# Kernel tuning notes

Hardware: AMD Instinct MI355X
Metric: run time of the kernel (lower is better)

The kernel has to match this reference:

```python
import jax, jax.numpy as jnp
import numpy as np

EPS = 1e-5

def _rms(t, w):
    # RMSNorm over last dim with learned scale w (broadcastable)
    return t * jax.lax.rsqrt(jnp.mean(t * t, axis=-1, keepdims=True) + EPS) * w

def setup_inputs() -> dict:
    key = jax.random.key(0)
    ks = jax.random.split(key, 8)
    B, S, D, H, HD, M = 2, 2048, 1024, 16, 64, 2
    E = H * HD
    sc = 0.02
    x = jax.random.normal(ks[0], (B, S, D), jnp.float32)
    attn_mask = jnp.zeros((S, S), jnp.float32)  # additive mask
    mod_ids = jax.random.randint(ks[1], (B, S), 0, M)
    Wq = jax.random.normal(ks[2], (M, D, E), jnp.float32) * sc
    Wk = jax.random.normal(ks[3], (M, D, E), jnp.float32) * sc
    Wv = jax.random.normal(ks[4], (M, D, E), jnp.float32) * sc
    Wo = jax.random.normal(ks[5], (M, E, D), jnp.float32) * sc
    qn_w = jnp.ones((M, HD), jnp.float32)
    kn_w = jnp.ones((M, HD), jnp.float32)
    attn_norm_w = jnp.ones((M, D), jnp.float32)
    return {"x": x, "attn_mask": attn_mask, "mod_ids": mod_ids,
            "Wq": Wq, "Wk": Wk, "Wv": Wv, "Wo": Wo,
            "qn_w": qn_w, "kn_w": kn_w, "attn_norm_w": attn_norm_w}

def reference(x, attn_mask, mod_ids, Wq, Wk, Wv, Wo, qn_w, kn_w, attn_norm_w):
    B, S, D = x.shape
    M = Wq.shape[0]
    HD = qn_w.shape[-1]
    E = Wq.shape[-1]
    H = E // HD
    msk = jax.nn.one_hot(mod_ids, M, dtype=x.dtype)  # [B,S,M] one-hot routing

    # modality-expert QKV projections: [M,B,S,E]
    q_m = jnp.einsum('bsd,mde->mbse', x, Wq).reshape(M, B, S, H, HD)
    k_m = jnp.einsum('bsd,mde->mbse', x, Wk).reshape(M, B, S, H, HD)
    v_m = jnp.einsum('bsd,mde->mbse', x, Wv)
    # per-modality, per-head QK RMSNorm
    q_m = _rms(q_m, qn_w[:, None, None, None, :]).reshape(M, B, S, E)
    k_m = _rms(k_m, kn_w[:, None, None, None, :]).reshape(M, B, S, E)

    # merge modalities (scatter by routing mask)
    q = jnp.einsum('bsm,mbse->bse', msk, q_m).reshape(B, S, H, HD)
    k = jnp.einsum('bsm,mbse->bse', msk, k_m).reshape(B, S, H, HD)
    v = jnp.einsum('bsm,mbse->bse', msk, v_m).reshape(B, S, H, HD)

    # standard multi-head attention
    scores = jnp.einsum('bqhd,bkhd->bhqk', q, k) / jnp.sqrt(jnp.asarray(HD, x.dtype))
    scores = scores + attn_mask  # additive mask broadcast over [B,H]
    attn = jax.nn.softmax(scores, axis=-1)
    ctx = jnp.einsum('bhqk,bkhd->bqhd', attn, v).reshape(B, S, E)
    attn_weights = attn.mean(axis=1)  # [B,S,S], averaged over heads

    # modality-expert output projection + RMSNorm, scatter-merge back
    o_m = jnp.einsum('bse,med->mbsd', ctx, Wo)
    o_m = _rms(o_m, attn_norm_w[:, None, None, :])
    out = jnp.einsum('bsm,mbsd->bsd', msk, o_m)
    return out, attn_weights
```

## Files before the change

kernel.cpp:

```cpp
#include <hip/hip_runtime.h>
#include <cstdint>

#define Bc  2
#define Sc  2048
#define Dc  1024
#define Ec  1024
#define Hc  16
#define HDc 64
#define TTc (Bc*Sc)
#define TILE_R 128
#define NTILES 36
#define EPSc 1e-5f
#define LOG2E 1.44269504f
#define C2    (0.125f*LOG2E)

typedef unsigned short u16;
using bf8   = __attribute__((ext_vector_type(8))) short;
using f32x4 = __attribute__((ext_vector_type(4))) float;
#define MFMA(a,b,c) __builtin_amdgcn_mfma_f32_16x16x32_bf16(a,b,c,0,0,0)

static __device__ __forceinline__ u16 f2b(float f){
    return (u16)((__float_as_uint(f) + 0x8000u) >> 16);
}
static __device__ __forceinline__ float b2f(u16 s){
    return __uint_as_float(((unsigned)s) << 16);
}
static __device__ __forceinline__ float ex2(float x){
    return __builtin_amdgcn_exp2f(x);
}
static __device__ __forceinline__ unsigned cvtpk(float a, float b){
    unsigned r;
    asm("v_cvt_pk_bf16_f32 %0, %1, %2" : "=v"(r) : "v"(a), "v"(b));
    return r;
}
union bfpack { unsigned u[4]; bf8 v; };
static __device__ __forceinline__ float max3f(float a, float b, float c){
    return fmaxf(fmaxf(a, b), c);
}
static __device__ __forceinline__ u16* swz(u16* base, int row, int col8){
    return base + row*64 + ((col8 ^ (row & 7)) << 3);
}
static __device__ __forceinline__ const u16* swzc(const u16* base, int row, int col8){
    return base + row*64 + ((col8 ^ (row & 7)) << 3);
}
typedef const __attribute__((address_space(1))) void* gp1;
typedef __attribute__((address_space(3))) void* lp3;
static __device__ __forceinline__ void gl16(const void* g, void* l){
    __builtin_amdgcn_global_load_lds((gp1)g, (lp3)l, 16, 0, 0);
}
static __device__ __forceinline__ int pinv(int lr){
    return (lr & 0x23) | ((lr & 0x10) >> 2) | ((lr & 0x0C) << 1);
}

__global__ void k_perm(const int* __restrict__ mod, int* __restrict__ perm,
                       int* __restrict__ tmeta, u16* __restrict__ zbuf)
{
    __shared__ int cnt[4], segstart[4];
    int t = threadIdx.x;
    for (int i = t; i < 2048; i += 256) zbuf[i] = 0;
    if (t < 4) cnt[t] = 0;
    __syncthreads();
    for (int i = t; i < TTc; i += 256){
        int b = i >> 11; int m = mod[i];
        atomicAdd(&cnt[b*2+m], 1);
    }
    __syncthreads();
    if (t == 0){
        int off = 0;
        for (int i = 0; i < 4; i++){
            segstart[i] = off;
            int pad = ((cnt[i] + TILE_R - 1)/TILE_R)*TILE_R;
            for (int tt = off/TILE_R; tt < (off+pad)/TILE_R; tt++) tmeta[tt] = i;
            off += pad;
        }
        for (int tt = off/TILE_R; tt < NTILES; tt++) tmeta[tt] = -1;
    }
    __syncthreads();
    if (t < 4) cnt[t] = 0;
    for (int i = t; i < NTILES*TILE_R; i += 256) perm[i] = -1;
    __syncthreads();
    for (int i = t; i < TTc; i += 256){
        int b = i >> 11, s = i & 2047; int m = mod[i];
        int r = atomicAdd(&cnt[b*2+m], 1);
        perm[segstart[b*2+m] + r] = s;
    }
}

__global__ __launch_bounds__(256) void k_prep(
    const float* __restrict__ x, const float* __restrict__ mask,
    u16* __restrict__ xb, u16* __restrict__ maskb)
{
    int bid = blockIdx.x;
    if (bid < 4096){
        int i = (bid*256 + threadIdx.x)*4;
        float4 v = *(const float4*)&x[i];
        ushort4 o;
        o.x = f2b(v.x); o.y = f2b(v.y); o.z = f2b(v.z); o.w = f2b(v.w);
        *(ushort4*)&xb[i] = o;
    } else {
        int i = ((bid-4096)*256 + threadIdx.x)*4;
        float4 v = *(const float4*)&mask[i];
        ushort4 o;
        o.x = f2b(v.x*LOG2E); o.y = f2b(v.y*LOG2E);
        o.z = f2b(v.z*LOG2E); o.w = f2b(v.w*LOG2E);
        *(ushort4*)&maskb[i] = o;
    }
}

__global__ __launch_bounds__(256) void k_tcvt(
    const float* __restrict__ s0, const float* __restrict__ s1,
    const float* __restrict__ s2, const float* __restrict__ s3,
    u16* __restrict__ d0, u16* __restrict__ d1,
    u16* __restrict__ d2, u16* __restrict__ d3)
{
    int wsel = blockIdx.z >> 1, m = blockIdx.z & 1;
    const float* src = (wsel==0?s0:wsel==1?s1:wsel==2?s2:s3) + (size_t)m*1048576;
    u16*       dst = (wsel==0?d0:wsel==1?d1:wsel==2?d2:d3) + (size_t)m*1048576;
    __shared__ float sh[32][33];
    int t = threadIdx.x;
    int i0 = blockIdx.x*32, j0 = blockIdx.y*32;
    {
        int i = t >> 3, j4 = (t & 7)*4;
        *(float4*)&sh[i][j4] = *(const float4*)&src[(size_t)(i0+i)*1024 + j0 + j4];
    }
    __syncthreads();
    {
        int j = t >> 3, i4 = (t & 7)*4;
        ushort4 o;
        o.x = f2b(sh[i4+0][j]); o.y = f2b(sh[i4+1][j]);
        o.z = f2b(sh[i4+2][j]); o.w = f2b(sh[i4+3][j]);
        *(ushort4*)&dst[(size_t)(j0+j)*1024 + i0 + i4] = o;
    }
}

__global__ __launch_bounds__(256) void k_qkv(
    const u16* __restrict__ xb, const u16* __restrict__ wqT,
    const u16* __restrict__ wkT, const u16* __restrict__ wvT,
    const int* __restrict__ perm, const int* __restrict__ tmeta,
    const float* __restrict__ qnw, const float* __restrict__ knw,
    const u16* __restrict__ zbuf,
    u16* __restrict__ qb, u16* __restrict__ kb, u16* __restrict__ vb)
{
    int meta = tmeta[blockIdx.y];
    if (meta < 0) return;
    int b = meta >> 1, m = meta & 1;
    const u16* W = (blockIdx.z==0 ? wqT : (blockIdx.z==1 ? wkT : wvT)) + (size_t)m*Ec*Dc;
    u16* outp    = (blockIdx.z==0 ? qb  : (blockIdx.z==1 ? kb  : vb));
    int c0 = blockIdx.x*128;
    int t = threadIdx.x, lane = t & 63, wv_ = t >> 6;
    int quad = lane >> 4, lc = lane & 15;

    __shared__ u16 at[128*64];
    __shared__ u16 bt[128*64];
    __shared__ int sperm[128];
    if (t < 128) sperm[t] = perm[blockIdx.y*128 + t];
    f32x4 acc[2][8];
    #pragma unroll
    for (int i=0;i<2;i++)
        #pragma unroll
        for (int j=0;j<8;j++) acc[i][j] = (f32x4){0.f,0.f,0.f,0.f};
    __syncthreads();

    int colsw = ((lane & 7) ^ (lane >> 3)) << 3;
    const u16* ab[4]; const u16* bb[4];
    #pragma unroll
    for (int i = 0; i < 4; i++){
        int row = wv_*32 + i*8 + (lane >> 3);
        int s_ = sperm[row];
        ab[i] = (s_ >= 0) ? (xb + ((size_t)(b*Sc + s_))*Dc + colsw) : zbuf;
        bb[i] = W + (size_t)(c0 + row)*Dc + colsw;
    }

    for (int d0 = 0; d0 < Dc; d0 += 64){
        #pragma unroll
        for (int i = 0; i < 4; i++){
            gl16(ab[i] + d0, &at[(wv_*4 + i)*512]);
            gl16(bb[i] + d0, &bt[(wv_*4 + i)*512]);
        }
        __syncthreads();
        #pragma unroll
        for (int ks = 0; ks < 2; ks++){
            bf8 a0 = *(const bf8*)swzc(at, wv_*32 + lc,      ks*4 + quad);
            bf8 a1 = *(const bf8*)swzc(at, wv_*32 + 16 + lc, ks*4 + quad);
            #pragma unroll
            for (int nb = 0; nb < 8; nb++){
                bf8 bb2 = *(const bf8*)swzc(bt, nb*16 + lc, ks*4 + quad);
                acc[0][nb] = MFMA(a0, bb2, acc[0][nb]);
                acc[1][nb] = MFMA(a1, bb2, acc[1][nb]);
            }
        }
        __syncthreads();
    }

    if (blockIdx.z < 2){
        const float* nw = (blockIdx.z==0 ? qnw : knw) + m*HDc;
        float cs = (blockIdx.z==0) ? C2 : 1.f;
        float w0 = nw[lc]*cs, w1 = nw[16+lc]*cs, w2 = nw[32+lc]*cs, w3 = nw[48+lc]*cs;
        #pragma unroll
        for (int mb = 0; mb < 2; mb++){
            #pragma unroll
            for (int r = 0; r < 4; r++){
                #pragma unroll
                for (int g = 0; g < 2; g++){
                    float ss = 0.f;
                    #pragma unroll
                    for (int j = 0; j < 4; j++){
                        float v2 = acc[mb][g*4+j][r];
                        ss += v2*v2;
                    }
                    ss += __shfl_xor(ss, 1, 64);
                    ss += __shfl_xor(ss, 2, 64);
                    ss += __shfl_xor(ss, 4, 64);
                    ss += __shfl_xor(ss, 8, 64);
                    float rs = rsqrtf(ss*(1.f/64.f) + EPSc);
                    acc[mb][g*4+0][r] *= rs*w0;
                    acc[mb][g*4+1][r] *= rs*w1;
                    acc[mb][g*4+2][r] *= rs*w2;
                    acc[mb][g*4+3][r] *= rs*w3;
                }
            }
        }
    }

    int h0 = c0 >> 6;
    #pragma unroll
    for (int mb = 0; mb < 2; mb++){
        #pragma unroll
        for (int r = 0; r < 4; r++){
            int row = wv_*32 + mb*16 + quad*4 + r;
            int s_ = sperm[row];
            if (s_ < 0) continue;
            #pragma unroll
            for (int nb = 0; nb < 8; nb++){
                int col = nb*16 + lc;
                int h = h0 + (col >> 6), hd = col & 63;
                outp[(((size_t)(b*Hc + h))*Sc + s_)*HDc + hd] = f2b(acc[mb][nb][r]);
            }
        }
    }
}

__global__ __launch_bounds__(256) void k_vt(const u16* __restrict__ vb,
                                            u16* __restrict__ vtb)
{
    __shared__ u16 sh[64][72];
    int t = threadIdx.x;
    int s0 = blockIdx.x*64, bh = blockIdx.y;
    {
        int rr = t >> 2, cc = (t & 3)*16;
        const u16* src = vb + ((size_t)bh*Sc + s0 + rr)*HDc + cc;
        *(uint4*)&sh[rr][cc]   = *(const uint4*)(src);
        *(uint4*)&sh[rr][cc+8] = *(const uint4*)(src+8);
    }
    __syncthreads();
    {
        int hd = t >> 2, sc = (t & 3)*16;
        u16 tmp[16];
        #pragma unroll
        for (int j = 0; j < 16; j++) tmp[j] = sh[sc+j][hd];
        u16* dst = vtb + ((size_t)bh*HDc + hd)*Sc + s0 + sc;
        *(uint4*)(dst)   = *(const uint4*)&tmp[0];
        *(uint4*)(dst+8) = *(const uint4*)&tmp[8];
    }
}

__global__ __launch_bounds__(256) void k_flash(
    const u16* __restrict__ qb, const u16* __restrict__ kb,
    const u16* __restrict__ vtb, const u16* __restrict__ maskb,
    float* __restrict__ pm, float* __restrict__ pl,
    u16* __restrict__ c0, u16* __restrict__ c1)
{
    int qs0 = blockIdx.x*64, h = blockIdx.y;
    int b = blockIdx.z >> 1, half = blockIdx.z & 1;
    u16* ctxh = half ? c1 : c0;
    int t = threadIdx.x, lane = t & 63, wv_ = t >> 6;
    int quad = lane >> 4, lc = lane & 15;
    __shared__ u16 kt[2][64*64];
    __shared__ u16 vt[2][64*64];
    const u16* qp  = qb  + ((size_t)(b*Hc+h))*Sc*HDc;
    const u16* kp  = kb  + ((size_t)(b*Hc+h))*Sc*HDc;
    const u16* vtp = vtb + ((size_t)(b*Hc+h))*HDc*Sc;
    const u16* mq  = maskb + (size_t)(qs0 + wv_*16 + lc)*Sc;
    bf8 aq[2];
    #pragma unroll
    for (int ks = 0; ks < 2; ks++)
        aq[ks] = *(const bf8*)(qp + (size_t)(qs0 + wv_*16 + lc)*HDc + ks*32 + quad*8);
    bfpack onep; onep.u[0] = onep.u[1] = onep.u[2] = onep.u[3] = 0x3F803F80u;
    bf8 ones = onep.v;
    float rm = -1.0e30f;
    f32x4 racc = (f32x4){0.f,0.f,0.f,0.f};
    f32x4 oacc[4];
    #pragma unroll
    for (int j=0;j<4;j++) oacc[j] = (f32x4){0.f,0.f,0.f,0.f};

    int lsub = lane >> 3;
    int colsw = ((lane & 7) ^ lsub) << 3;
    int lrA = wv_*16 + lsub, lrB = wv_*16 + 8 + lsub;
    const u16* kg0 = kp + (size_t)pinv(lrA)*HDc + colsw;
    const u16* kg1 = kp + (size_t)pinv(lrB)*HDc + colsw;
    const u16* vg0 = vtp + (size_t)lrA*Sc + colsw;
    const u16* vg1 = vtp + (size_t)lrB*Sc + colsw;
    int kdo0 = (wv_*16 + 0)*64, kdo1 = (wv_*16 + 8)*64;

    int kc0 = half*1024, kcend = kc0 + 1024;
    gl16(kg0 + (size_t)kc0*HDc, &kt[0][kdo0]);
    gl16(kg1 + (size_t)kc0*HDc, &kt[0][kdo1]);
    gl16(vg0 + kc0, &vt[0][kdo0]);
    gl16(vg1 + kc0, &vt[0][kdo1]);
    ushort4 mv[2][2];
    #pragma unroll
    for (int a1 = 0; a1 < 2; a1++)
        #pragma unroll
        for (int b1 = 0; b1 < 2; b1++)
            mv[a1][b1] = *(const ushort4*)(mq + kc0 + a1*32 + quad*8 + b1*4);
    __syncthreads();

    int cur = 0;
    for (int kc = kc0; kc < kcend; kc += 64){
        int nxt = (kc + 64 < kcend) ? kc + 64 : kc;
        gl16(kg0 + (size_t)nxt*HDc, &kt[cur^1][kdo0]);
        gl16(kg1 + (size_t)nxt*HDc, &kt[cur^1][kdo1]);
        gl16(vg0 + nxt, &vt[cur^1][kdo0]);
        gl16(vg1 + nxt, &vt[cur^1][kdo1]);
        ushort4 mvn[2][2];
        #pragma unroll
        for (int a1 = 0; a1 < 2; a1++)
            #pragma unroll
            for (int b1 = 0; b1 < 2; b1++)
                mvn[a1][b1] = *(const ushort4*)(mq + nxt + a1*32 + quad*8 + b1*4);

        const u16* ktc = kt[cur];
        const u16* vtc = vt[cur];
        f32x4 acc[4];
        #pragma unroll
        for (int j=0;j<4;j++) acc[j] = (f32x4){0.f,0.f,0.f,0.f};
        #pragma unroll
        for (int ks = 0; ks < 2; ks++){
            #pragma unroll
            for (int nb = 0; nb < 4; nb++){
                bf8 ak = *(const bf8*)swzc(ktc, nb*16 + lc, ks*4 + quad);
                acc[nb] = MFMA(ak, aq[ks], acc[nb]);
            }
        }
        float svv[4][4];
        #pragma unroll
        for (int a1 = 0; a1 < 2; a1++){
            #pragma unroll
            for (int b1 = 0; b1 < 2; b1++){
                int nb = 2*a1 + b1;
                #pragma unroll
                for (int r = 0; r < 4; r++){
                    u16 mraw = (r==0?mv[a1][b1].x:r==1?mv[a1][b1].y:
                                r==2?mv[a1][b1].z:mv[a1][b1].w);
                    svv[nb][r] = acc[nb][r] + b2f(mraw);
                }
            }
        }
        float m0_ = max3f(svv[0][0], svv[0][1], svv[0][2]);
        float m1_ = max3f(svv[0][3], svv[1][0], svv[1][1]);
        float m2_ = max3f(svv[1][2], svv[1][3], svv[2][0]);
        float m3_ = max3f(svv[2][1], svv[2][2], svv[2][3]);
        float m4_ = max3f(svv[3][0], svv[3][1], svv[3][2]);
        float mxl = fmaxf(max3f(m0_, m1_, m2_), max3f(m3_, m4_, svv[3][3]));
        if (__any(mxl > rm + 8.f)){
            float mx = fmaxf(mxl, __shfl_xor(mxl, 16, 64));
            mx = fmaxf(mx, __shfl_xor(mx, 32, 64));
            float nm = fmaxf(rm, mx);
            float fac = ex2(rm - nm);
            rm = nm;
            float f0 = __shfl(fac, quad*4+0, 64);
            float f1 = __shfl(fac, quad*4+1, 64);
            float f2 = __shfl(fac, quad*4+2, 64);
            float f3 = __shfl(fac, quad*4+3, 64);
            racc[0] *= f0; racc[1] *= f1; racc[2] *= f2; racc[3] *= f3;
            #pragma unroll
            for (int nb = 0; nb < 4; nb++){
                oacc[nb][0] *= f0; oacc[nb][1] *= f1;
                oacc[nb][2] *= f2; oacc[nb][3] *= f3;
            }
        }
        #pragma unroll
        for (int a1 = 0; a1 < 2; a1++){
            bfpack pk;
            pk.u[0] = cvtpk(ex2(svv[2*a1][0] - rm),   ex2(svv[2*a1][1] - rm));
            pk.u[1] = cvtpk(ex2(svv[2*a1][2] - rm),   ex2(svv[2*a1][3] - rm));
            pk.u[2] = cvtpk(ex2(svv[2*a1+1][0] - rm), ex2(svv[2*a1+1][1] - rm));
            pk.u[3] = cvtpk(ex2(svv[2*a1+1][2] - rm), ex2(svv[2*a1+1][3] - rm));
            bf8 ap = pk.v;
            racc = MFMA(ap, ones, racc);
            #pragma unroll
            for (int nb2 = 0; nb2 < 4; nb2++){
                bf8 bv = *(const bf8*)swzc(vtc, nb2*16 + lc, a1*4 + quad);
                oacc[nb2] = MFMA(ap, bv, oacc[nb2]);
            }
        }
        __syncthreads();
        #pragma unroll
        for (int a1 = 0; a1 < 2; a1++)
            #pragma unroll
            for (int b1 = 0; b1 < 2; b1++)
                mv[a1][b1] = mvn[a1][b1];
        cur ^= 1;
    }
    size_t sbase = (size_t)half*65536 + ((size_t)(b*Hc+h))*Sc + qs0 + wv_*16;
    if (quad == 0) pm[sbase + lc] = rm;
    if (lc == 0){
        #pragma unroll
        for (int r = 0; r < 4; r++) pl[sbase + quad*4 + r] = racc[r];
    }
    #pragma unroll
    for (int r = 0; r < 4; r++){
        float ir = 1.f/racc[r];
        int tok = qs0 + wv_*16 + quad*4 + r;
        #pragma unroll
        for (int nb = 0; nb < 4; nb++){
            int hd = nb*16 + lc;
            ctxh[((size_t)(b*Sc + tok))*Ec + h*HDc + hd] = f2b(oacc[nb][r]*ir);
        }
    }
}

__global__ __launch_bounds__(256) void k_merge(
    const float* __restrict__ pm, const float* __restrict__ pl,
    float* __restrict__ lstc, float* __restrict__ w0, float* __restrict__ w1)
{
    int r = blockIdx.x*256 + threadIdx.x;
    float m0 = pm[r],        m1 = pm[65536 + r];
    float l0 = pl[r],        l1 = pl[65536 + r];
    float M  = fmaxf(m0, m1);
    float e0 = ex2(m0 - M)*l0;
    float e1 = ex2(m1 - M)*l1;
    float L  = e0 + e1;
    float iL = 1.f/L;
    lstc[r] = M + log2f(L);
    w0[r] = e0*iL;
    w1[r] = e1*iL;
}

__global__ __launch_bounds__(256) void k_addc(u16* __restrict__ c0,
                                              const u16* __restrict__ c1,
                                              const float* __restrict__ w0,
                                              const float* __restrict__ w1)
{
    int i = (blockIdx.x*256 + threadIdx.x)*8;
    int hh = (i >> 6) & 15, s = (i >> 10) & 2047, bb = i >> 21;
    int wi = ((bb*Hc + hh) << 11) + s;
    float wa = w0[wi], wb = w1[wi];
    ushort4 a0 = *(ushort4*)&c0[i],   a1 = *(ushort4*)&c0[i+4];
    ushort4 b0 = *(const ushort4*)&c1[i], b1 = *(const ushort4*)&c1[i+4];
    ushort4 o0, o1;
    o0.x = f2b(b2f(a0.x)*wa + b2f(b0.x)*wb); o0.y = f2b(b2f(a0.y)*wa + b2f(b0.y)*wb);
    o0.z = f2b(b2f(a0.z)*wa + b2f(b0.z)*wb); o0.w = f2b(b2f(a0.w)*wa + b2f(b0.w)*wb);
    o1.x = f2b(b2f(a1.x)*wa + b2f(b1.x)*wb); o1.y = f2b(b2f(a1.y)*wa + b2f(b1.y)*wb);
    o1.z = f2b(b2f(a1.z)*wa + b2f(b1.z)*wb); o1.w = f2b(b2f(a1.w)*wa + b2f(b1.w)*wb);
    *(ushort4*)&c0[i]   = o0;
    *(ushort4*)&c0[i+4] = o1;
}

__global__ __launch_bounds__(256) void k_attnw(
    const u16* __restrict__ qb, const u16* __restrict__ kb,
    const u16* __restrict__ maskb, const float* __restrict__ lstc,
    float* __restrict__ awout)
{
    int qs0 = blockIdx.x*64, ks0 = blockIdx.y*64, b = blockIdx.z;
    int t = threadIdx.x, lane = t & 63, wv_ = t >> 6;
    int quad = lane >> 4, lc = lane & 15;
    __shared__ u16 kt[64*64];
    __shared__ float scc[64];
    f32x4 T[4];
    #pragma unroll
    for (int j=0;j<4;j++) T[j] = (f32x4){0.f,0.f,0.f,0.f};

    int lsub = lane >> 3;
    int colsw = ((lane & 7) ^ lsub) << 3;
    int lrA = wv_*16 + lsub, lrB = wv_*16 + 8 + lsub;
    u16* kd0 = &kt[(wv_*16 + 0)*64];
    u16* kd1 = &kt[(wv_*16 + 8)*64];

    for (int h = 0; h < Hc; h++){
        __syncthreads();
        const u16* qp = qb + ((size_t)(b*Hc+h))*Sc*HDc;
        const u16* kp = kb + ((size_t)(b*Hc+h))*Sc*HDc;
        bf8 aq[2];
        #pragma unroll
        for (int ks = 0; ks < 2; ks++)
            aq[ks] = *(const bf8*)(qp + (size_t)(qs0 + wv_*16 + lc)*HDc + ks*32 + quad*8);
        gl16(kp + (size_t)(ks0 + lrA)*HDc + colsw, kd0);
        gl16(kp + (size_t)(ks0 + lrB)*HDc + colsw, kd1);
        if (t < 64)
            scc[t] = lstc[((size_t)(b*Hc+h))*Sc + qs0 + t];
        __syncthreads();
        f32x4 acc[4];
        #pragma unroll
        for (int j=0;j<4;j++) acc[j] = (f32x4){0.f,0.f,0.f,0.f};
        #pragma unroll
        for (int ks = 0; ks < 2; ks++){
            #pragma unroll
            for (int nb = 0; nb < 4; nb++){
                bf8 bb = *(const bf8*)swzc(kt, nb*16 + lc, ks*4 + quad);
                acc[nb] = MFMA(aq[ks], bb, acc[nb]);
            }
        }
        #pragma unroll
        for (int r = 0; r < 4; r++){
            int row = wv_*16 + quad*4 + r;
            float cv = scc[row];
            #pragma unroll
            for (int nb = 0; nb < 4; nb++)
                T[nb][r] += ex2(acc[nb][r] - cv);
        }
    }
    #pragma unroll
    for (int r = 0; r < 4; r++){
        int gq = qs0 + wv_*16 + quad*4 + r;
        #pragma unroll
        for (int nb = 0; nb < 4; nb++){
            int gk = ks0 + nb*16 + lc;
            float mk = b2f(maskb[(size_t)gq*Sc + gk]);
            awout[(size_t)b*Sc*Sc + (size_t)gq*Sc + gk]
                = T[nb][r]*ex2(mk)*(1.f/16.f);
        }
    }
}

__global__ __launch_bounds__(256) void k_oproj(
    const u16* __restrict__ ctxb, const u16* __restrict__ woT,
    const int* __restrict__ perm, const int* __restrict__ tmeta,
    const u16* __restrict__ zbuf, float* __restrict__ opre)
{
    int meta = tmeta[blockIdx.y];
    if (meta < 0) return;
    int b = meta >> 1, m = meta & 1;
    const u16* W = woT + (size_t)m*Ec*Dc;
    int c0 = blockIdx.x*128;
    int t = threadIdx.x, lane = t & 63, wv_ = t >> 6;
    int quad = lane >> 4, lc = lane & 15;
    __shared__ u16 at[128*64];
    __shared__ u16 bt[128*64];
    __shared__ int sperm[128];
    if (t < 128) sperm[t] = perm[blockIdx.y*128 + t];
    f32x4 acc[2][8];
    #pragma unroll
    for (int i=0;i<2;i++)
        #pragma unroll
        for (int j=0;j<8;j++) acc[i][j] = (f32x4){0.f,0.f,0.f,0.f};
    __syncthreads();

    int colsw = ((lane & 7) ^ (lane >> 3)) << 3;
    const u16* ab[4]; const u16* bb[4];
    #pragma unroll
    for (int i = 0; i < 4; i++){
        int row = wv_*32 + i*8 + (lane >> 3);
        int s_ = sperm[row];
        ab[i] = (s_ >= 0) ? (ctxb + ((size_t)(b*Sc + s_))*Ec + colsw) : zbuf;
        bb[i] = W + (size_t)(c0 + row)*Ec + colsw;
    }

    for (int d0 = 0; d0 < Ec; d0 += 64){
        #pragma unroll
        for (int i = 0; i < 4; i++){
            gl16(ab[i] + d0, &at[(wv_*4 + i)*512]);
            gl16(bb[i] + d0, &bt[(wv_*4 + i)*512]);
        }
        __syncthreads();
        #pragma unroll
        for (int ks = 0; ks < 2; ks++){
            bf8 a0 = *(const bf8*)swzc(at, wv_*32 + lc,      ks*4 + quad);
            bf8 a1 = *(const bf8*)swzc(at, wv_*32 + 16 + lc, ks*4 + quad);
            #pragma unroll
            for (int nb = 0; nb < 8; nb++){
                bf8 bb2 = *(const bf8*)swzc(bt, nb*16 + lc, ks*4 + quad);
                acc[0][nb] = MFMA(a0, bb2, acc[0][nb]);
                acc[1][nb] = MFMA(a1, bb2, acc[1][nb]);
            }
        }
        __syncthreads();
    }
    #pragma unroll
    for (int mb = 0; mb < 2; mb++){
        #pragma unroll
        for (int r = 0; r < 4; r++){
            int row = wv_*32 + mb*16 + quad*4 + r;
            int s_ = sperm[row];
            if (s_ < 0) continue;
            #pragma unroll
            for (int nb = 0; nb < 8; nb++){
                int col = c0 + nb*16 + lc;
                opre[((size_t)(b*Sc + s_))*Dc + col] = acc[mb][nb][r];
            }
        }
    }
}

__global__ __launch_bounds__(256) void k_onorm(
    const float* __restrict__ opre, const float* __restrict__ anw,
    const int* __restrict__ mod, float* __restrict__ out)
{
    int row = blockIdx.x;
    int m = mod[row];
    int t = threadIdx.x;
    float val[4];
    float ss = 0.f;
    #pragma unroll
    for (int j=0;j<4;j++){
        val[j] = opre[(size_t)row*Dc + t + 256*j];
        ss += val[j]*val[j];
    }
    #pragma unroll
    for (int o=32;o>0;o>>=1) ss += __shfl_xor(ss, o, 64);
    __shared__ float red[4];
    int wid = t>>6, lane = t&63;
    if (lane==0) red[wid]=ss;
    __syncthreads();
    float tot = red[0]+red[1]+red[2]+red[3];
    float rms = rsqrtf(tot*(1.f/1024.f) + EPSc);
    #pragma unroll
    for (int j=0;j<4;j++)
        out[(size_t)row*Dc + t + 256*j] = val[j]*rms*anw[m*Dc + t + 256*j];
}

extern "C" void kernel_launch(void* const* d_in, const int* in_sizes, int n_in,
                              void* d_out, int out_size, void* d_ws, size_t ws_size,
                              hipStream_t stream)
{
    const float* x    = (const float*)d_in[0];
    const float* mask = (const float*)d_in[1];
    const int*   mod  = (const int*)  d_in[2];
    const float* Wq   = (const float*)d_in[3];
    const float* Wk   = (const float*)d_in[4];
    const float* Wv   = (const float*)d_in[5];
    const float* Wo   = (const float*)d_in[6];
    const float* qnw  = (const float*)d_in[7];
    const float* knw  = (const float*)d_in[8];
    const float* anw  = (const float*)d_in[9];

    float* out   = (float*)d_out;
    float* awout = out + (size_t)Bc*Sc*Dc;

    float* ws = (float*)d_ws;
    u16* qb    = (u16*)(ws + 0);
    u16* kb    = (u16*)(ws + 2097152);
    u16* vb    = (u16*)(ws + 4194304);
    u16* xb    = (u16*)(ws + 6291456);
    u16* ctx0  = xb;
    u16* ctx1  = vb;
    u16* vtb   = (u16*)(ws + 8388608);
    u16* wqT   = (u16*)(ws + 10485760);
    u16* wkT   = (u16*)(ws + 11534336);
    u16* wvT   = (u16*)(ws + 12582912);
    u16* woT   = (u16*)(ws + 13631488);
    float* lstc= ws + 14680064;
    float* pm  = ws + 14811136;
    float* pl  = pm + 131072;
    float* w0  = ws + 15073280;
    float* w1  = w0 + 65536;
    u16* maskb = (u16*)(ws + 15335424);
    int* perm  = (int*)(ws + 17432576);
    int* tmeta = perm + NTILES*TILE_R;
    u16* zbuf  = (u16*)(tmeta + NTILES + 28);
    float* opre = ws;

    k_perm  <<<dim3(1),            256, 0, stream>>>(mod, perm, tmeta, zbuf);
    k_prep  <<<dim3(8192),         256, 0, stream>>>(x, mask, xb, maskb);
    k_tcvt  <<<dim3(32,32,8),      256, 0, stream>>>(Wq, Wk, Wv, Wo, wqT, wkT, wvT, woT);
    k_qkv   <<<dim3(8,NTILES,3),   256, 0, stream>>>(xb, wqT, wkT, wvT, perm, tmeta,
                                                     qnw, knw, zbuf, qb, kb, vb);
    k_vt    <<<dim3(32,32),        256, 0, stream>>>(vb, vtb);
    k_flash <<<dim3(32,16,4),      256, 0, stream>>>(qb, kb, vtb, maskb, pm, pl, ctx0, ctx1);
    k_merge <<<dim3(256),          256, 0, stream>>>(pm, pl, lstc, w0, w1);
    k_attnw <<<dim3(32,32,2),      256, 0, stream>>>(qb, kb, maskb, lstc, awout);
    k_addc  <<<dim3(2048),         256, 0, stream>>>(ctx0, ctx1, w0, w1);
    k_oproj <<<dim3(8,NTILES),     256, 0, stream>>>(ctx0, woT, perm, tmeta, zbuf, opre);
    k_onorm <<<dim3(4096),         256, 0, stream>>>(opre, anw, mod, out);
}
```

Before: 345.7 us.

## Drop split-KV flash attention, process full key range per block

Flash attention previously split the key range into two halves across blocks, then needed a merge kernel for the softmax stats and an add kernel to combine the two partial contexts. Each block now walks all 2048 keys, writes the log-sum-exp directly and emits the final normalized context, which removes two kernel launches and the partial-result round trips to memory. The cost is half as many blocks (1024 instead of 2048) and twice as long a serial loop per block, which reduces parallelism and latency hiding on a large GPU.

```diff
diff --git a/kernel.cpp b/kernel.cpp
--- a/kernel.cpp
+++ b/kernel.cpp
@@ -267,12 +267,10 @@
 __global__ __launch_bounds__(256) void k_flash(
     const u16* __restrict__ qb, const u16* __restrict__ kb,
     const u16* __restrict__ vtb, const u16* __restrict__ maskb,
-    float* __restrict__ pm, float* __restrict__ pl,
-    u16* __restrict__ c0, u16* __restrict__ c1)
+    float* __restrict__ lstc, u16* __restrict__ c0)
 {
     int qs0 = blockIdx.x*64, h = blockIdx.y;
-    int b = blockIdx.z >> 1, half = blockIdx.z & 1;
-    u16* ctxh = half ? c1 : c0;
+    int b = blockIdx.z;
     int t = threadIdx.x, lane = t & 63, wv_ = t >> 6;
     int quad = lane >> 4, lc = lane & 15;
     __shared__ u16 kt[2][64*64];
@@ -302,22 +300,21 @@
     const u16* vg1 = vtp + (size_t)lrB*Sc + colsw;
     int kdo0 = (wv_*16 + 0)*64, kdo1 = (wv_*16 + 8)*64;
 
-    int kc0 = half*1024, kcend = kc0 + 1024;
-    gl16(kg0 + (size_t)kc0*HDc, &kt[0][kdo0]);
-    gl16(kg1 + (size_t)kc0*HDc, &kt[0][kdo1]);
-    gl16(vg0 + kc0, &vt[0][kdo0]);
-    gl16(vg1 + kc0, &vt[0][kdo1]);
+    gl16(kg0, &kt[0][kdo0]);
+    gl16(kg1, &kt[0][kdo1]);
+    gl16(vg0, &vt[0][kdo0]);
+    gl16(vg1, &vt[0][kdo1]);
     ushort4 mv[2][2];
     #pragma unroll
     for (int a1 = 0; a1 < 2; a1++)
         #pragma unroll
         for (int b1 = 0; b1 < 2; b1++)
-            mv[a1][b1] = *(const ushort4*)(mq + kc0 + a1*32 + quad*8 + b1*4);
+            mv[a1][b1] = *(const ushort4*)(mq + a1*32 + quad*8 + b1*4);
     __syncthreads();
 
     int cur = 0;
-    for (int kc = kc0; kc < kcend; kc += 64){
-        int nxt = (kc + 64 < kcend) ? kc + 64 : kc;
+    for (int kc = 0; kc < Sc; kc += 64){
+        int nxt = (kc + 64 < Sc) ? kc + 64 : kc;
         gl16(kg0 + (size_t)nxt*HDc, &kt[cur^1][kdo0]);
         gl16(kg1 + (size_t)nxt*HDc, &kt[cur^1][kdo1]);
         gl16(vg0 + nxt, &vt[cur^1][kdo0]);
@@ -402,11 +399,14 @@
                 mv[a1][b1] = mvn[a1][b1];
         cur ^= 1;
     }
-    size_t sbase = (size_t)half*65536 + ((size_t)(b*Hc+h))*Sc + qs0 + wv_*16;
-    if (quad == 0) pm[sbase + lc] = rm;
+    float rmr[4];
+    #pragma unroll
+    for (int r = 0; r < 4; r++) rmr[r] = __shfl(rm, quad*4 + r, 64);
+    size_t sbase = ((size_t)(b*Hc+h))*Sc + qs0 + wv_*16;
     if (lc == 0){
         #pragma unroll
-        for (int r = 0; r < 4; r++) pl[sbase + quad*4 + r] = racc[r];
+        for (int r = 0; r < 4; r++)
+            lstc[sbase + quad*4 + r] = rmr[r] + log2f(racc[r]);
     }
     #pragma unroll
     for (int r = 0; r < 4; r++){
@@ -415,46 +415,9 @@
         #pragma unroll
         for (int nb = 0; nb < 4; nb++){
             int hd = nb*16 + lc;
-            ctxh[((size_t)(b*Sc + tok))*Ec + h*HDc + hd] = f2b(oacc[nb][r]*ir);
-        }
-    }
-}
-
-__global__ __launch_bounds__(256) void k_merge(
-    const float* __restrict__ pm, const float* __restrict__ pl,
-    float* __restrict__ lstc, float* __restrict__ w0, float* __restrict__ w1)
-{
-    int r = blockIdx.x*256 + threadIdx.x;
-    float m0 = pm[r],        m1 = pm[65536 + r];
-    float l0 = pl[r],        l1 = pl[65536 + r];
-    float M  = fmaxf(m0, m1);
-    float e0 = ex2(m0 - M)*l0;
-    float e1 = ex2(m1 - M)*l1;
-    float L  = e0 + e1;
-    float iL = 1.f/L;
-    lstc[r] = M + log2f(L);
-    w0[r] = e0*iL;
-    w1[r] = e1*iL;
-}
-
-__global__ __launch_bounds__(256) void k_addc(u16* __restrict__ c0,
-                                              const u16* __restrict__ c1,
-                                              const float* __restrict__ w0,
-                                              const float* __restrict__ w1)
-{
-    int i = (blockIdx.x*256 + threadIdx.x)*8;
-    int hh = (i >> 6) & 15, s = (i >> 10) & 2047, bb = i >> 21;
-    int wi = ((bb*Hc + hh) << 11) + s;
-    float wa = w0[wi], wb = w1[wi];
-    ushort4 a0 = *(ushort4*)&c0[i],   a1 = *(ushort4*)&c0[i+4];
-    ushort4 b0 = *(const ushort4*)&c1[i], b1 = *(const ushort4*)&c1[i+4];
-    ushort4 o0, o1;
-    o0.x = f2b(b2f(a0.x)*wa + b2f(b0.x)*wb); o0.y = f2b(b2f(a0.y)*wa + b2f(b0.y)*wb);
-    o0.z = f2b(b2f(a0.z)*wa + b2f(b0.z)*wb); o0.w = f2b(b2f(a0.w)*wa + b2f(b0.w)*wb);
-    o1.x = f2b(b2f(a1.x)*wa + b2f(b1.x)*wb); o1.y = f2b(b2f(a1.y)*wa + b2f(b1.y)*wb);
-    o1.z = f2b(b2f(a1.z)*wa + b2f(b1.z)*wb); o1.w = f2b(b2f(a1.w)*wa + b2f(b1.w)*wb);
-    *(ushort4*)&c0[i]   = o0;
-    *(ushort4*)&c0[i+4] = o1;
+            c0[((size_t)(b*Sc + tok))*Ec + h*HDc + hd] = f2b(oacc[nb][r]*ir);
+        }
+    }
 }
 
 __global__ __launch_bounds__(256) void k_attnw(
@@ -643,17 +606,12 @@
     u16* vb    = (u16*)(ws + 4194304);
     u16* xb    = (u16*)(ws + 6291456);
     u16* ctx0  = xb;
-    u16* ctx1  = vb;
     u16* vtb   = (u16*)(ws + 8388608);
     u16* wqT   = (u16*)(ws + 10485760);
     u16* wkT   = (u16*)(ws + 11534336);
     u16* wvT   = (u16*)(ws + 12582912);
     u16* woT   = (u16*)(ws + 13631488);
     float* lstc= ws + 14680064;
-    float* pm  = ws + 14811136;
-    float* pl  = pm + 131072;
-    float* w0  = ws + 15073280;
-    float* w1  = w0 + 65536;
     u16* maskb = (u16*)(ws + 15335424);
     int* perm  = (int*)(ws + 17432576);
     int* tmeta = perm + NTILES*TILE_R;
@@ -666,10 +624,8 @@
     k_qkv   <<<dim3(8,NTILES,3),   256, 0, stream>>>(xb, wqT, wkT, wvT, perm, tmeta,
                                                      qnw, knw, zbuf, qb, kb, vb);
     k_vt    <<<dim3(32,32),        256, 0, stream>>>(vb, vtb);
-    k_flash <<<dim3(32,16,4),      256, 0, stream>>>(qb, kb, vtb, maskb, pm, pl, ctx0, ctx1);
-    k_merge <<<dim3(256),          256, 0, stream>>>(pm, pl, lstc, w0, w1);
+    k_flash <<<dim3(32,16,2),      256, 0, stream>>>(qb, kb, vtb, maskb, lstc, ctx0);
     k_attnw <<<dim3(32,32,2),      256, 0, stream>>>(qb, kb, maskb, lstc, awout);
-    k_addc  <<<dim3(2048),         256, 0, stream>>>(ctx0, ctx1, w0, w1);
     k_oproj <<<dim3(8,NTILES),     256, 0, stream>>>(ctx0, woT, perm, tmeta, zbuf, opre);
     k_onorm <<<dim3(4096),         256, 0, stream>>>(opre, anw, mod, out);
 }
```

Result: faster. 338.6 us (-2.1%).
